# Optimization experiments

Measured on AMD Instinct MI355X. Metric: run time of the kernel, lower is better.

## Reference

```python
import jax, jax.numpy as jnp
import numpy as np

K, F = 1025, 8192  # zonotope error terms (+center) and feature width


def setup_inputs() -> dict:
    key = jax.random.key(0)
    k1, k2 = jax.random.split(key)
    x = jax.random.normal(k1, (K, F), dtype=jnp.float32)
    lambdas = jax.random.uniform(k2, (1, F), dtype=jnp.float32)  # learnable slopes in [0,1]
    return {"x": x, "lambdas": lambdas}


def reference(x, lambdas):
    # x: [K, F] zonotope (row 0 = center, rows 1: = error terms)
    f = x.shape[1]
    abssum = jnp.sum(jnp.abs(x[1:]), axis=0)          # [F]
    l = x[0] - abssum                                 # lower bound
    u = x[0] + abssum                                 # upper bound
    pos = (l > 0).astype(x.dtype)                     # heaviside(l)
    cross = ((u > 0) & (l < 0)).astype(x.dtype)       # heaviside(u)*heaviside(-l)
    lam = lambdas[0]                                  # [F]
    d = jnp.maximum(-l * lam, u * (1.0 - lam))        # relaxation offset
    scale = pos + cross * lam                         # fused per-feature scale
    out = scale[None, :] * x                          # [K, F]
    half = 0.5 * cross * d                            # [F]
    out = out.at[0].add(half)                         # shift center
    # extend_Z: one new error-term row per crossing ReLU. Padded (jit-static)
    # version: F rows, row i = e_i * d_i/2 where crossing, zero otherwise.
    idx = jnp.arange(f)
    ext = jnp.zeros((f, f), dtype=x.dtype).at[idx, idx].set(half)
    return jnp.concatenate([out, ext], axis=0)        # [K+F, F]
```

## Files before the change

### kernel.cpp

```cpp
#include <hip/hip_runtime.h>


#define BLK 256

__global__ void k_partial_abssum(const float4* __restrict__ x4,
                                 float4* __restrict__ partial4,
                                 int f4, int rows, int rpc) {
    int col4  = blockIdx.x * BLK + threadIdx.x;
    int chunk = blockIdx.y;
    int r0 = chunk * rpc;
    int r1 = r0 + rpc;
    if (r1 > rows) r1 = rows;
    float4 s = make_float4(0.f, 0.f, 0.f, 0.f);
    for (int r = r0; r < r1; ++r) {
        float4 v = x4[(size_t)(1 + r) * f4 + col4];
        s.x += fabsf(v.x);
        s.y += fabsf(v.y);
        s.z += fabsf(v.z);
        s.w += fabsf(v.w);
    }
    partial4[(size_t)chunk * f4 + col4] = s;
}

__global__ void k_finalize(const float* __restrict__ partial,
                           int chunks,
                           const float* __restrict__ x,
                           const float* __restrict__ lambdas,
                           float* __restrict__ scale,
                           float* __restrict__ half_,
                           int F) {
    int col = blockIdx.x * BLK + threadIdx.x;
    if (col >= F) return;
    float s = 0.f;
    for (int c = 0; c < chunks; ++c)
        s += partial[(size_t)c * F + col];
    float cen = x[col];
    float l = cen - s;
    float u = cen + s;
    float la = lambdas[col];
    float pos   = (l > 0.f) ? 1.f : 0.f;
    float cross = (u > 0.f && l < 0.f) ? 1.f : 0.f;
    float d = fmaxf(-l * la, u * (1.f - la));
    scale[col] = pos + cross * la;
    half_[col] = 0.5f * cross * d;
}

__global__ void k_scale_rows(const float4* __restrict__ x4,
                             const float4* __restrict__ scale4,
                             const float4* __restrict__ half4,
                             float4* __restrict__ out4,
                             int f4) {
    int col4 = blockIdx.x * BLK + threadIdx.x;
    int row  = blockIdx.y;
    float4 v = x4[(size_t)row * f4 + col4];
    float4 s = scale4[col4];
    float4 o;
    o.x = v.x * s.x;
    o.y = v.y * s.y;
    o.z = v.z * s.z;
    o.w = v.w * s.w;
    if (row == 0) {
        float4 h = half4[col4];
        o.x += h.x; o.y += h.y; o.z += h.z; o.w += h.w;
    }
    out4[(size_t)row * f4 + col4] = o;
}

__global__ void k_write_ext(float4* __restrict__ ext4,
                            const float* __restrict__ half_,
                            int f4) {
    int row   = blockIdx.x;
    int diag4 = row >> 2;
    int lane  = row & 3;
    float hv  = half_[row];
    size_t base = (size_t)row * f4;
    for (int c4 = threadIdx.x; c4 < f4; c4 += BLK) {
        float4 z = make_float4(0.f, 0.f, 0.f, 0.f);
        if (c4 == diag4) {
            ((float*)&z)[lane] = hv;
        }
        ext4[base + c4] = z;
    }
}

extern "C" void kernel_launch(void* const* d_in, const int* in_sizes, int n_in,
                              void* d_out, int out_size, void* d_ws, size_t ws_size,
                              hipStream_t stream) {
    const float* x       = (const float*)d_in[0];
    const float* lambdas = (const float*)d_in[1];

    const int F    = in_sizes[1];
    const int K    = in_sizes[0] / F;
    const int f4   = F / 4;
    const int rows = K - 1;

    const int CHUNKS = 64;
    const int rpc = (rows + CHUNKS - 1) / CHUNKS;

    float* wsf     = (float*)d_ws;
    float* half_   = wsf;
    float* scale   = wsf + F;
    float* partial = wsf + 2 * (size_t)F;

    float* out = (float*)d_out;
    float* ext = out + (size_t)K * F;

    const float4* x4 = (const float4*)x;

    k_partial_abssum<<<dim3(f4 / BLK, CHUNKS), BLK, 0, stream>>>(
        x4, (float4*)partial, f4, rows, rpc);

    k_finalize<<<dim3((F + BLK - 1) / BLK), BLK, 0, stream>>>(
        partial, CHUNKS, x, lambdas, scale, half_, F);

    k_scale_rows<<<dim3(f4 / BLK, K), BLK, 0, stream>>>(
        x4, (const float4*)scale, (const float4*)half_, (float4*)out, f4);

    k_write_ext<<<dim3(F), BLK, 0, stream>>>(
        (float4*)ext, half_, f4);
}
```

Baseline: 357.4 us.

## Zero extension block via hipMemsetAsync and use nontemporal stores for scaled rows

Replaces the custom kernel that wrote the F×F extension block (zeros plus a diagonal) with a hipMemsetAsync zero-fill followed by a small kernel that writes only the diagonal. The memset is issued first so the runtime's optimized fill path can do the bulk 256MB write. The scaled-row kernel now uses nontemporal vector stores so output does not pollute caches. Risks: the memset path may not beat a well-vectorized store kernel, and it adds an extra launch.

Measured after the change: 341.3 us. 4.5% less time.

```diff
diff --git a/kernel.cpp b/kernel.cpp
--- a/kernel.cpp
+++ b/kernel.cpp
@@ -2,6 +2,8 @@
 
 
 #define BLK 256
+
+typedef float v4f __attribute__((ext_vector_type(4)));
 
 __global__ void k_partial_abssum(const float4* __restrict__ x4,
                                  float4* __restrict__ partial4,
@@ -48,13 +50,13 @@
 __global__ void k_scale_rows(const float4* __restrict__ x4,
                              const float4* __restrict__ scale4,
                              const float4* __restrict__ half4,
-                             float4* __restrict__ out4,
+                             v4f* __restrict__ out4,
                              int f4) {
     int col4 = blockIdx.x * BLK + threadIdx.x;
     int row  = blockIdx.y;
     float4 v = x4[(size_t)row * f4 + col4];
     float4 s = scale4[col4];
-    float4 o;
+    v4f o;
     o.x = v.x * s.x;
     o.y = v.y * s.y;
     o.z = v.z * s.z;
@@ -63,23 +65,15 @@
         float4 h = half4[col4];
         o.x += h.x; o.y += h.y; o.z += h.z; o.w += h.w;
     }
-    out4[(size_t)row * f4 + col4] = o;
+    __builtin_nontemporal_store(o, &out4[(size_t)row * f4 + col4]);
 }
 
-__global__ void k_write_ext(float4* __restrict__ ext4,
-                            const float* __restrict__ half_,
-                            int f4) {
-    int row   = blockIdx.x;
-    int diag4 = row >> 2;
-    int lane  = row & 3;
-    float hv  = half_[row];
-    size_t base = (size_t)row * f4;
-    for (int c4 = threadIdx.x; c4 < f4; c4 += BLK) {
-        float4 z = make_float4(0.f, 0.f, 0.f, 0.f);
-        if (c4 == diag4) {
-            ((float*)&z)[lane] = hv;
-        }
-        ext4[base + c4] = z;
+__global__ void k_diag(float* __restrict__ ext,
+                       const float* __restrict__ half_,
+                       int F) {
+    int i = blockIdx.x * BLK + threadIdx.x;
+    if (i < F) {
+        ext[(size_t)i * F + i] = half_[i];
     }
 }
 
@@ -107,6 +101,8 @@
 
     const float4* x4 = (const float4*)x;
 
+    (void)hipMemsetAsync(ext, 0, (size_t)F * F * sizeof(float), stream);
+
     k_partial_abssum<<<dim3(f4 / BLK, CHUNKS), BLK, 0, stream>>>(
         x4, (float4*)partial, f4, rows, rpc);
 
@@ -114,8 +110,7 @@
         partial, CHUNKS, x, lambdas, scale, half_, F);
 
     k_scale_rows<<<dim3(f4 / BLK, K), BLK, 0, stream>>>(
-        x4, (const float4*)scale, (const float4*)half_, (float4*)out, f4);
+        x4, (const float4*)scale, (const float4*)half_, (v4f*)out, f4);
 
-    k_write_ext<<<dim3(F), BLK, 0, stream>>>(
-        (float4*)ext, half_, f4);
+    k_diag<<<dim3((F + BLK - 1) / BLK), BLK, 0, stream>>>(ext, half_, F);
 }
```
